# Kernel optimization log

Measured on AMD Instinct MI355X. Metric: run time of the kernel, lower is better.

## Reference

```python
import jax, jax.numpy as jnp
import numpy as np

MODEL_BATCHES = 2048
NUM_POINTS = 8192
N_FUNCS = 8
REMOVE_ITERS = 51  # remove_points = 51 * model_batches -> first 51 iterations dropped


def setup_inputs() -> dict:
    key = jax.random.key(0)
    k1, k2, k3, k4, k5 = jax.random.split(key, 5)
    point = jax.random.normal(k1, (MODEL_BATCHES, 2, 1), dtype=jnp.float32) * 0.1
    optimized_weights = jax.random.normal(k2, (N_FUNCS, 2, 2), dtype=jnp.float32) * 0.5
    optimized_biases = jax.random.normal(k3, (N_FUNCS, 2, 1), dtype=jnp.float32) * 0.5
    optimized_function_ops = jax.random.uniform(k4, (N_FUNCS,), dtype=jnp.float32)
    index = jax.random.randint(k5, (MODEL_BATCHES, NUM_POINTS), 0, N_FUNCS, dtype=jnp.int32)
    return {
        "point": point,
        "optimized_weights": optimized_weights,
        "optimized_biases": optimized_biases,
        "optimized_function_ops": optimized_function_ops,
        "index": index,
    }


def reference(point, optimized_weights, optimized_biases, optimized_function_ops, index):
    mb = point.shape[0]

    def step(p, idx):  # p: [mb,2,1], idx: [mb]
        W = optimized_weights[idx]          # [mb,2,2]
        b = optimized_biases[idx]           # [mb,2,1]
        op = optimized_function_ops[idx]    # [mb]
        p_new = jnp.einsum('bij,bjk->bik', W, p) + b  # [mb,2,1]
        out = jnp.concatenate([p_new[:, :, 0], op[:, None]], axis=1)  # [mb,3]
        return p_new, out

    # scan over iterations: index.T is [num_points, mb]
    _, outs = jax.lax.scan(step, point, index.T)  # outs: [num_points, mb, 3]
    pts = outs.reshape(-1, 3)  # matches torch.cat along dim 0 then squeeze
    return pts[REMOVE_ITERS * mb:, :]
```

## Files before the change

### kernel.cpp

```cpp
#include <hip/hip_runtime.h>
#include <hip/hip_fp16.h>

#define MB   2048
#define NP   8192
#define NF   8
#define RM   51
#define NCH  64
#define CH   128

typedef float        f32x4 __attribute__((ext_vector_type(4)));
typedef unsigned int u32;


__device__ __forceinline__ void build_tbl(u32 (*tbl)[4], const float* W,
                                          const float* B, const float* OPS, int tid)
{
    if (tid < NF) {
        const __half2 h0 = __floats2half2_rn(W[tid*4+0], W[tid*4+1]);
        const __half2 h1 = __floats2half2_rn(W[tid*4+2], W[tid*4+3]);
        const __half2 h2 = __floats2half2_rn(B[tid*2+0], B[tid*2+1]);
        const __half2 h3 = __floats2half2_rn(OPS ? OPS[tid] : 0.f, 0.f);
        tbl[tid][0] = __builtin_bit_cast(u32, h0);
        tbl[tid][1] = __builtin_bit_cast(u32, h1);
        tbl[tid][2] = __builtin_bit_cast(u32, h2);
        tbl[tid][3] = __builtin_bit_cast(u32, h3);
    }
}

__global__ __launch_bounds__(256, 4) void ifs_phase1(
    const int* __restrict__ idxg, const float* __restrict__ W,
    const float* __restrict__ B,
    float4* __restrict__ mapsA, float2* __restrict__ mapsC)
{
    __shared__ u32 ptile[256][33];
    __shared__ __align__(16) u32 tbl[NF][4];
    const int tid = threadIdx.x;
    build_tbl(tbl, W, B, nullptr, tid);

    const int c  = blockIdx.x >> 3;
    const int b0 = (blockIdx.x & 7) << 8;
    const int x8 = tid & 7, yy = tid >> 3;

    auto stage = [&](int seg) {
        #pragma unroll
        for (int p = 0; p < 8; ++p) {
            const int row = yy + p * 32;
            const int4 v = *(const int4*)(idxg + (size_t)(b0 + row) * NP
                                          + c * CH + seg * 32 + x8 * 4);
            ptile[row][seg * 8 + x8] =
                (u32)v.x | ((u32)v.y << 8) | ((u32)v.z << 16) | ((u32)v.w << 24);
        }
    };
    stage(0);
    __syncthreads();

    float a00 = 1.f, a01 = 0.f, a10 = 0.f, a11 = 1.f, c0 = 0.f, c1 = 0.f;
    for (int seg = 0; seg < 4; ++seg) {
        if (seg < 3) stage(seg + 1);
        #pragma unroll
        for (int j = 0; j < 8; ++j) {
            const u32 pc = ptile[tid][seg * 8 + j];
            #pragma unroll
            for (int e = 0; e < 4; ++e) {
                const int f = (pc >> (8 * e)) & 7;
                const uint4 u = *(const uint4*)&tbl[f][0];
                const float2 w0 = __half22float2(__builtin_bit_cast(__half2, u.x));
                const float2 w1 = __half22float2(__builtin_bit_cast(__half2, u.y));
                const float2 bb = __half22float2(__builtin_bit_cast(__half2, u.z));
                const float na00 = w0.x*a00 + w0.y*a10;
                const float na01 = w0.x*a01 + w0.y*a11;
                const float na10 = w1.x*a00 + w1.y*a10;
                const float na11 = w1.x*a01 + w1.y*a11;
                const float nc0  = w0.x*c0  + w0.y*c1 + bb.x;
                const float nc1  = w1.x*c0  + w1.y*c1 + bb.y;
                a00 = na00; a01 = na01; a10 = na10; a11 = na11; c0 = nc0; c1 = nc1;
            }
        }
        __syncthreads();
    }
    mapsA[(size_t)c * MB + b0 + tid] = make_float4(a00, a01, a10, a11);
    mapsC[(size_t)c * MB + b0 + tid] = make_float2(c0, c1);
}

__global__ __launch_bounds__(64) void ifs_phase2(
    const float2* __restrict__ point, const float4* __restrict__ mapsA,
    const float2* __restrict__ mapsC, float2* __restrict__ pe)
{
    const int b = blockIdx.x * 64 + threadIdx.x;
    float2 p = point[b];
    float4 A0[8], A1[8]; float2 C0[8], C1[8];
    #pragma unroll
    for (int k = 0; k < 8; ++k) {
        A0[k] = mapsA[(size_t)k * MB + b];
        C0[k] = mapsC[(size_t)k * MB + b];
    }
    for (int g = 0; g < 8; ++g) {
        if (g < 7) {
            #pragma unroll
            for (int k = 0; k < 8; ++k) {
                A1[k] = mapsA[(size_t)((g + 1) * 8 + k) * MB + b];
                C1[k] = mapsC[(size_t)((g + 1) * 8 + k) * MB + b];
            }
        }
        #pragma unroll
        for (int k = 0; k < 8; ++k) {
            pe[(size_t)(g * 8 + k) * MB + b] = p;
            const float nx = A0[k].x * p.x + A0[k].y * p.y + C0[k].x;
            const float ny = A0[k].z * p.x + A0[k].w * p.y + C0[k].y;
            p.x = nx; p.y = ny;
        }
        #pragma unroll
        for (int k = 0; k < 8; ++k) { A0[k] = A1[k]; C0[k] = C1[k]; }
    }
}

__global__ __launch_bounds__(256, 2) void ifs_phase3(
    const int* __restrict__ idxg, const float* __restrict__ W,
    const float* __restrict__ B, const float* __restrict__ OPS,
    const float2* __restrict__ pe, float* __restrict__ out)
{
    __shared__ u32 ptile[256][33];
    __shared__ __align__(16) float sbuf[2][4][256][4];
    __shared__ __align__(16) u32 tbl[NF][4];
    const int tid = threadIdx.x;
    build_tbl(tbl, W, B, OPS, tid);

    const int c  = blockIdx.x >> 3;
    const int b0 = (blockIdx.x & 7) << 8;
    const int x8 = tid & 7, yy = tid >> 3;

    auto stage = [&](int seg) {
        #pragma unroll
        for (int p = 0; p < 8; ++p) {
            const int row = yy + p * 32;
            const int4 v = *(const int4*)(idxg + (size_t)(b0 + row) * NP
                                          + c * CH + seg * 32 + x8 * 4);
            ptile[row][seg * 8 + x8] =
                (u32)v.x | ((u32)v.y << 8) | ((u32)v.z << 16) | ((u32)v.w << 24);
        }
    };
    stage(0);

    float2 p = pe[(size_t)c * MB + b0 + tid];

    int s_[3], r_[3];
    #pragma unroll
    for (int k = 0; k < 3; ++k) {
        const int w = 4 * (tid + 256 * k);
        s_[k] = w / 768;
        r_[k] = w - s_[k] * 768;
    }
    long long off[3];
    #pragma unroll
    for (int k = 0; k < 3; ++k)
        off[k] = (long long)(c * CH + s_[k] - RM) * (MB * 3) + b0 * 3 + r_[k];

    const bool chk = (c == 0);
    __syncthreads();

    for (int span = 0; span < 4; ++span) {
        if (span < 3) stage(span + 1);
        #pragma unroll
        for (int g = 0; g < 8; ++g) {
            const int buf = g & 1;
            const u32 pc = ptile[tid][span * 8 + g];
            #pragma unroll
            for (int s = 0; s < 4; ++s) {
                const int f = (pc >> (8 * s)) & 7;
                const uint4 u = *(const uint4*)&tbl[f][0];
                const float2 w0 = __half22float2(__builtin_bit_cast(__half2, u.x));
                const float2 w1 = __half22float2(__builtin_bit_cast(__half2, u.y));
                const float2 bb = __half22float2(__builtin_bit_cast(__half2, u.z));
                const float op  = __low2float(__builtin_bit_cast(__half2, u.w));
                const float nx = w0.x * p.x + w0.y * p.y + bb.x;
                const float ny = w1.x * p.x + w1.y * p.y + bb.y;
                p.x = nx; p.y = ny;
                f32x4 o4 = {nx, ny, op, 0.f};
                *(f32x4*)&sbuf[buf][s][tid][0] = o4;
            }
            __syncthreads();
            const int t0 = span * 32 + g * 4;
            const float* flat = &sbuf[buf][0][0][0];
            #pragma unroll
            for (int k = 0; k < 3; ++k) {
                if (!chk || (t0 + s_[k]) >= RM) {
                    const int w = 4 * (tid + 256 * k) - 768 * s_[k];
                    const int b1 = w / 3, cm0 = w - b1 * 3;
                    const float* row = flat + s_[k] * 1024;
                    f32x4 v;
                    int bb_ = b1, cc_ = cm0;
                    #pragma unroll
                    for (int j = 0; j < 4; ++j) {
                        v[j] = row[bb_ * 4 + cc_];
                        if (++cc_ == 3) { cc_ = 0; ++bb_; }
                    }
                    __builtin_nontemporal_store(v, (f32x4*)(out + off[k]));
                }
                off[k] += 4LL * (MB * 3);
            }
        }
    }
}

extern "C" void kernel_launch(void* const* d_in, const int* in_sizes, int n_in,
                              void* d_out, int out_size, void* d_ws, size_t ws_size,
                              hipStream_t stream) {
    const float* point = (const float*)d_in[0];
    const float* W     = (const float*)d_in[1];
    const float* B     = (const float*)d_in[2];
    const float* OPS   = (const float*)d_in[3];
    const int*   idx   = (const int*)  d_in[4];
    float*       out   = (float*)d_out;

    char* ws = (char*)d_ws;
    float4* mapsA = (float4*)(ws);
    float2* mapsC = (float2*)(ws + (size_t)NCH * MB * 16);
    float2* pe    = (float2*)(ws + (size_t)NCH * MB * 24);

    ifs_phase1<<<NCH * (MB / 256), 256, 0, stream>>>(idx, W, B, mapsA, mapsC);
    ifs_phase2<<<MB / 64, 64, 0, stream>>>((const float2*)point, mapsA, mapsC, pe);
    ifs_phase3<<<NCH * (MB / 256), 256, 0, stream>>>(idx, W, B, OPS, pe, out);
}
```

Before: 72.91 us.

## Halve chunk length and pass packed index codes from phase1 to phase3

Chunks shrink from 128 to 64 steps, so the grid doubles to 128 chunks and phase2 runs 16 groups instead of 8. Phase1 now writes its byte-packed index codes to workspace, and phase3 reads those compact codes instead of re-reading the full int32 index array. Phase3 also stores outputs as packed 3-float rows in shared memory, so it reads float4 vectors directly rather than gathering them, and it targets occupancy 4. The cost is a longer serial phase2 plus extra workspace traffic for the codes and maps.

```diff
diff --git a/kernel.cpp b/kernel.cpp
--- a/kernel.cpp
+++ b/kernel.cpp
@@ -5,8 +5,9 @@
 #define NP   8192
 #define NF   8
 #define RM   51
-#define NCH  64
-#define CH   128
+#define NCH  128
+#define CH   64
+#define NW   16
 
 typedef float        f32x4 __attribute__((ext_vector_type(4)));
 typedef unsigned int u32;
@@ -30,9 +31,9 @@
 __global__ __launch_bounds__(256, 4) void ifs_phase1(
     const int* __restrict__ idxg, const float* __restrict__ W,
     const float* __restrict__ B,
-    float4* __restrict__ mapsA, float2* __restrict__ mapsC)
-{
-    __shared__ u32 ptile[256][33];
+    float4* __restrict__ mapsA, float2* __restrict__ mapsC, u32* __restrict__ codes)
+{
+    __shared__ u32 ptile[256][NW + 1];
     __shared__ __align__(16) u32 tbl[NF][4];
     const int tid = threadIdx.x;
     build_tbl(tbl, W, B, nullptr, tid);
@@ -55,8 +56,8 @@
     __syncthreads();
 
     float a00 = 1.f, a01 = 0.f, a10 = 0.f, a11 = 1.f, c0 = 0.f, c1 = 0.f;
-    for (int seg = 0; seg < 4; ++seg) {
-        if (seg < 3) stage(seg + 1);
+    for (int seg = 0; seg < 2; ++seg) {
+        if (seg == 0) stage(1);
         #pragma unroll
         for (int j = 0; j < 8; ++j) {
             const u32 pc = ptile[tid][seg * 8 + j];
@@ -78,6 +79,9 @@
         }
         __syncthreads();
     }
+    #pragma unroll
+    for (int w = 0; w < NW; ++w)
+        codes[((size_t)c * NW + w) * MB + b0 + tid] = ptile[tid][w];
     mapsA[(size_t)c * MB + b0 + tid] = make_float4(a00, a01, a10, a11);
     mapsC[(size_t)c * MB + b0 + tid] = make_float2(c0, c1);
 }
@@ -94,8 +98,8 @@
         A0[k] = mapsA[(size_t)k * MB + b];
         C0[k] = mapsC[(size_t)k * MB + b];
     }
-    for (int g = 0; g < 8; ++g) {
-        if (g < 7) {
+    for (int g = 0; g < 16; ++g) {
+        if (g < 15) {
             #pragma unroll
             for (int k = 0; k < 8; ++k) {
                 A1[k] = mapsA[(size_t)((g + 1) * 8 + k) * MB + b];
@@ -114,90 +118,66 @@
     }
 }
 
-__global__ __launch_bounds__(256, 2) void ifs_phase3(
-    const int* __restrict__ idxg, const float* __restrict__ W,
+__global__ __launch_bounds__(256, 4) void ifs_phase3(
+    const u32* __restrict__ codes, const float* __restrict__ W,
     const float* __restrict__ B, const float* __restrict__ OPS,
     const float2* __restrict__ pe, float* __restrict__ out)
 {
-    __shared__ u32 ptile[256][33];
-    __shared__ __align__(16) float sbuf[2][4][256][4];
+    __shared__ __align__(16) float sbuf[2][4][256][3];
     __shared__ __align__(16) u32 tbl[NF][4];
     const int tid = threadIdx.x;
     build_tbl(tbl, W, B, OPS, tid);
 
     const int c  = blockIdx.x >> 3;
     const int b0 = (blockIdx.x & 7) << 8;
-    const int x8 = tid & 7, yy = tid >> 3;
-
-    auto stage = [&](int seg) {
-        #pragma unroll
-        for (int p = 0; p < 8; ++p) {
-            const int row = yy + p * 32;
-            const int4 v = *(const int4*)(idxg + (size_t)(b0 + row) * NP
-                                          + c * CH + seg * 32 + x8 * 4);
-            ptile[row][seg * 8 + x8] =
-                (u32)v.x | ((u32)v.y << 8) | ((u32)v.z << 16) | ((u32)v.w << 24);
-        }
-    };
-    stage(0);
-
-    float2 p = pe[(size_t)c * MB + b0 + tid];
-
-    int s_[3], r_[3];
+    const int b  = b0 + tid;
+
+    u32 code[NW];
+    #pragma unroll
+    for (int w = 0; w < NW; ++w)
+        code[w] = codes[((size_t)c * NW + w) * MB + b];
+    const float2 p0 = pe[(size_t)c * MB + b];
+
+    int s_[3];
+    long long off[3];
     #pragma unroll
     for (int k = 0; k < 3; ++k) {
         const int w = 4 * (tid + 256 * k);
         s_[k] = w / 768;
-        r_[k] = w - s_[k] * 768;
-    }
-    long long off[3];
-    #pragma unroll
-    for (int k = 0; k < 3; ++k)
-        off[k] = (long long)(c * CH + s_[k] - RM) * (MB * 3) + b0 * 3 + r_[k];
-
+        const int r = w - s_[k] * 768;
+        off[k] = (long long)(c * CH + s_[k] - RM) * (MB * 3) + b0 * 3 + r;
+    }
     const bool chk = (c == 0);
+    float2 p = p0;
     __syncthreads();
 
-    for (int span = 0; span < 4; ++span) {
-        if (span < 3) stage(span + 1);
-        #pragma unroll
-        for (int g = 0; g < 8; ++g) {
-            const int buf = g & 1;
-            const u32 pc = ptile[tid][span * 8 + g];
-            #pragma unroll
-            for (int s = 0; s < 4; ++s) {
-                const int f = (pc >> (8 * s)) & 7;
-                const uint4 u = *(const uint4*)&tbl[f][0];
-                const float2 w0 = __half22float2(__builtin_bit_cast(__half2, u.x));
-                const float2 w1 = __half22float2(__builtin_bit_cast(__half2, u.y));
-                const float2 bb = __half22float2(__builtin_bit_cast(__half2, u.z));
-                const float op  = __low2float(__builtin_bit_cast(__half2, u.w));
-                const float nx = w0.x * p.x + w0.y * p.y + bb.x;
-                const float ny = w1.x * p.x + w1.y * p.y + bb.y;
-                p.x = nx; p.y = ny;
-                f32x4 o4 = {nx, ny, op, 0.f};
-                *(f32x4*)&sbuf[buf][s][tid][0] = o4;
+    for (int g = 0; g < 16; ++g) {
+        const int buf = g & 1;
+        const u32 pc = code[g];
+        #pragma unroll
+        for (int s = 0; s < 4; ++s) {
+            const int f = (pc >> (8 * s)) & 7;
+            const uint4 u = *(const uint4*)&tbl[f][0];
+            const float2 w0 = __half22float2(__builtin_bit_cast(__half2, u.x));
+            const float2 w1 = __half22float2(__builtin_bit_cast(__half2, u.y));
+            const float2 bb = __half22float2(__builtin_bit_cast(__half2, u.z));
+            const float op  = __low2float(__builtin_bit_cast(__half2, u.w));
+            const float nx = w0.x * p.x + w0.y * p.y + bb.x;
+            const float ny = w1.x * p.x + w1.y * p.y + bb.y;
+            p.x = nx; p.y = ny;
+            sbuf[buf][s][tid][0] = nx;
+            sbuf[buf][s][tid][1] = ny;
+            sbuf[buf][s][tid][2] = op;
+        }
+        __syncthreads();
+        const float* flat = &sbuf[buf][0][0][0];
+        #pragma unroll
+        for (int k = 0; k < 3; ++k) {
+            if (!chk || (g * 4 + s_[k]) >= RM) {
+                const f32x4 v = *(const f32x4*)(flat + 4 * (tid + 256 * k));
+                __builtin_nontemporal_store(v, (f32x4*)(out + off[k]));
             }
-            __syncthreads();
-            const int t0 = span * 32 + g * 4;
-            const float* flat = &sbuf[buf][0][0][0];
-            #pragma unroll
-            for (int k = 0; k < 3; ++k) {
-                if (!chk || (t0 + s_[k]) >= RM) {
-                    const int w = 4 * (tid + 256 * k) - 768 * s_[k];
-                    const int b1 = w / 3, cm0 = w - b1 * 3;
-                    const float* row = flat + s_[k] * 1024;
-                    f32x4 v;
-                    int bb_ = b1, cc_ = cm0;
-                    #pragma unroll
-                    for (int j = 0; j < 4; ++j) {
-                        v[j] = row[bb_ * 4 + cc_];
-                        if (++cc_ == 3) { cc_ = 0; ++bb_; }
-                    }
-                    __builtin_nontemporal_store(v, (f32x4*)(out + off[k]));
-                }
-                off[k] += 4LL * (MB * 3);
-            }
+            off[k] += 4LL * (MB * 3);
         }
     }
 }
@@ -216,8 +196,9 @@
     float4* mapsA = (float4*)(ws);
     float2* mapsC = (float2*)(ws + (size_t)NCH * MB * 16);
     float2* pe    = (float2*)(ws + (size_t)NCH * MB * 24);
-
-    ifs_phase1<<<NCH * (MB / 256), 256, 0, stream>>>(idx, W, B, mapsA, mapsC);
+    u32*    codes = (u32*)   (ws + (size_t)NCH * MB * 32);
+
+    ifs_phase1<<<NCH * (MB / 256), 256, 0, stream>>>(idx, W, B, mapsA, mapsC, codes);
     ifs_phase2<<<MB / 64, 64, 0, stream>>>((const float2*)point, mapsA, mapsC, pe);
-    ifs_phase3<<<NCH * (MB / 256), 256, 0, stream>>>(idx, W, B, OPS, pe, out);
-}
+    ifs_phase3<<<NCH * (MB / 256), 256, 0, stream>>>(codes, W, B, OPS, pe, out);
+}
```

Result: slower. 76.48 us (+4.9%).
